# Performance work log

Measured on AMD Instinct MI355X. Metric: run time of the kernel, lower is better.

## Reference

```python
import jax, jax.numpy as jnp
import numpy as np

B, E, T, N = 1024, 512, 8, 256


def setup_inputs() -> dict:
    key = jax.random.key(0)
    k1, k2, k3, k4 = jax.random.split(key, 4)
    weights = jax.random.uniform(k1, (T,), dtype=jnp.float32)  # one scalar per bond type
    bond_src = jax.random.randint(k2, (B, E), 0, N - 1, dtype=jnp.int32)  # raw i, offset +1 later
    bond_dst = jax.random.randint(k3, (B, E), 0, N - 1, dtype=jnp.int32)
    bond_type = jax.random.randint(k4, (B, E), 0, T, dtype=jnp.int32)
    return {"weights": weights, "bond_src": bond_src, "bond_dst": bond_dst,
            "bond_type": bond_type, "num_nodes": N}


def reference(weights, bond_src, bond_dst, bond_type, num_nodes):
    # Gather per-bond weight, then symmetric scatter into dense [B, N, N] adjacency.
    batch, n_edges = bond_src.shape
    w = weights[bond_type]                                  # [B, E] gather
    bidx = jnp.broadcast_to(jnp.arange(batch)[:, None], (batch, n_edges))
    src = bond_src + 1                                      # +1 node offset as in torch code
    dst = bond_dst + 1
    bond_matrix = jnp.zeros((batch, num_nodes, num_nodes), dtype=weights.dtype)
    bond_matrix = bond_matrix.at[bidx, src, dst].set(w)
    bond_matrix = bond_matrix.at[bidx, dst, src].set(w)
    return bond_matrix
```

## Files before the change

### kernel.cpp

```cpp
#include <hip/hip_runtime.h>


#define NB_E 512
#define NB_N 256
#define CH_ROWS 64
#define CH_WORDS (CH_ROWS * NB_N / 2)

typedef float v4f __attribute__((ext_vector_type(4)));

__device__ __forceinline__ void lds_max_u16(unsigned int* tab, int cell, unsigned int v16)
{
    unsigned int* w = tab + (cell >> 1);
    const int sh = (cell & 1) * 16;
    unsigned int old = *w;
    while (true) {
        const unsigned int cur = (old >> sh) & 0xFFFFu;
        if (cur >= v16) break;
        const unsigned int nw = (old & ~(0xFFFFu << sh)) | (v16 << sh);
        const unsigned int seen = atomicCAS(w, old, nw);
        if (seen == old) break;
        old = seen;
    }
}

__global__ __launch_bounds__(256) void BondWeight_41738492182540_kernel(
    const float* __restrict__ weights,
    const int*   __restrict__ bsrc,
    const int*   __restrict__ bdst,
    const int*   __restrict__ btyp,
    float*       __restrict__ out)
{
    __shared__ unsigned int seqtab[CH_WORDS];
    __shared__ float s_wt[8];

    const int b = blockIdx.x;
    const int t = threadIdx.x;

    if (t < 8) s_wt[t] = weights[t];

    const int ebase = b * NB_E;
    int row[4], col[4];
    unsigned int pk[4];
    #pragma unroll
    for (int i = 0; i < 2; ++i) {
        const int e  = t + 256 * i;
        const int s1 = bsrc[ebase + e] + 1;
        const int d1 = bdst[ebase + e] + 1;
        const unsigned int ty = (unsigned int)btyp[ebase + e] & 7u;
        row[2*i]   = s1; col[2*i]   = d1; pk[2*i]   = ((unsigned int)(e + 1) << 3) | ty;
        row[2*i+1] = d1; col[2*i+1] = s1; pk[2*i+1] = ((unsigned int)(NB_E + e + 1) << 3) | ty;
    }

    {
        uint4* tab4 = (uint4*)seqtab;
        #pragma unroll
        for (int k = 0; k < CH_WORDS / 4 / 256; ++k)
            tab4[t + 256 * k] = make_uint4(0u, 0u, 0u, 0u);
    }
    __syncthreads();

    float4* __restrict__ out4 = ((float4*)out) + (size_t)b * (NB_N * NB_N / 4);
    uint2*  __restrict__ tab2 = (uint2*)seqtab;

    for (int r0 = 0; r0 < NB_N; r0 += CH_ROWS) {
        #pragma unroll
        for (int i = 0; i < 4; ++i) {
            const int r = row[i] - r0;
            if (0 <= r && r < CH_ROWS)
                lds_max_u16(seqtab, r * NB_N + col[i], pk[i]);
        }
        __syncthreads();

        #pragma unroll
        for (int k = 0; k < (CH_ROWS * NB_N / 4) / 256; ++k) {
            const int i4 = t + 256 * k;
            const uint2 ab = tab2[i4];
            tab2[i4] = make_uint2(0u, 0u);
            v4f v;
            unsigned int p;
            p = ab.x & 0xFFFFu; v.x = p ? s_wt[p & 7u] : 0.0f;
            p = ab.x >> 16;     v.y = p ? s_wt[p & 7u] : 0.0f;
            p = ab.y & 0xFFFFu; v.z = p ? s_wt[p & 7u] : 0.0f;
            p = ab.y >> 16;     v.w = p ? s_wt[p & 7u] : 0.0f;
            *(v4f*)&out4[r0 * (NB_N / 4) + i4] = v;
        }
        __syncthreads();
    }
}

extern "C" void kernel_launch(void* const* d_in, const int* in_sizes, int n_in,
                              void* d_out, int out_size, void* d_ws, size_t ws_size,
                              hipStream_t stream) {
    const float* weights = (const float*)d_in[0];
    const int*   bsrc    = (const int*)d_in[1];
    const int*   bdst    = (const int*)d_in[2];
    const int*   btyp    = (const int*)d_in[3];
    float*       out     = (float*)d_out;

    const int nb = in_sizes[1] / NB_E;

    BondWeight_41738492182540_kernel<<<nb, 256, 0, stream>>>(
        weights, bsrc, bdst, btyp, out);
}
```

Measured before the change: 272.8 us.

## Split each batch's row chunks across four blocks instead of looping

Launches four blocks per batch, each handling one 64-row chunk of the adjacency matrix, instead of one block looping over four chunks. This increases the number of blocks in flight and removes the per-chunk syncs and the table re-clearing. Edge loads become int2 vector loads with a changed edge-to-thread mapping, and the sequence numbering is kept consistent so the last-write priority is preserved. The cost is that every block re-reads all of its batch's edges, so edge reads from global memory increase fourfold.

Measured after the change: 275.5 us. Within noise of the previous version (+1.0%).

```diff
diff --git a/kernel.cpp b/kernel.cpp
--- a/kernel.cpp
+++ b/kernel.cpp
@@ -33,23 +33,12 @@
     __shared__ unsigned int seqtab[CH_WORDS];
     __shared__ float s_wt[8];
 
-    const int b = blockIdx.x;
-    const int t = threadIdx.x;
+    const int bx = blockIdx.x;
+    const int b  = bx >> 2;
+    const int r0 = (bx & 3) * CH_ROWS;
+    const int t  = threadIdx.x;
 
     if (t < 8) s_wt[t] = weights[t];
-
-    const int ebase = b * NB_E;
-    int row[4], col[4];
-    unsigned int pk[4];
-    #pragma unroll
-    for (int i = 0; i < 2; ++i) {
-        const int e  = t + 256 * i;
-        const int s1 = bsrc[ebase + e] + 1;
-        const int d1 = bdst[ebase + e] + 1;
-        const unsigned int ty = (unsigned int)btyp[ebase + e] & 7u;
-        row[2*i]   = s1; col[2*i]   = d1; pk[2*i]   = ((unsigned int)(e + 1) << 3) | ty;
-        row[2*i+1] = d1; col[2*i+1] = s1; pk[2*i+1] = ((unsigned int)(NB_E + e + 1) << 3) | ty;
-    }
 
     {
         uint4* tab4 = (uint4*)seqtab;
@@ -57,34 +46,51 @@
         for (int k = 0; k < CH_WORDS / 4 / 256; ++k)
             tab4[t + 256 * k] = make_uint4(0u, 0u, 0u, 0u);
     }
+
+    const int2 s2 = ((const int2*)(bsrc + b * NB_E))[t];
+    const int2 d2 = ((const int2*)(bdst + b * NB_E))[t];
+    const int2 y2 = ((const int2*)(btyp + b * NB_E))[t];
+
+    int row[4], col[4];
+    unsigned int pk[4];
+    {
+        const int e0 = 2 * t, e1 = 2 * t + 1;
+        const int sa = s2.x + 1, da = d2.x + 1;
+        const int sb = s2.y + 1, db = d2.y + 1;
+        const unsigned int ta = (unsigned int)y2.x & 7u;
+        const unsigned int tb = (unsigned int)y2.y & 7u;
+        row[0] = sa; col[0] = da; pk[0] = ((unsigned int)(e0 + 1) << 3) | ta;
+        row[1] = sb; col[1] = db; pk[1] = ((unsigned int)(e1 + 1) << 3) | tb;
+        row[2] = da; col[2] = sa; pk[2] = ((unsigned int)(NB_E + e0 + 1) << 3) | ta;
+        row[3] = db; col[3] = sb; pk[3] = ((unsigned int)(NB_E + e1 + 1) << 3) | tb;
+    }
+
     __syncthreads();
 
-    float4* __restrict__ out4 = ((float4*)out) + (size_t)b * (NB_N * NB_N / 4);
-    uint2*  __restrict__ tab2 = (uint2*)seqtab;
+    #pragma unroll
+    for (int i = 0; i < 4; ++i) {
+        const int r = row[i] - r0;
+        if (0 <= r && r < CH_ROWS)
+            lds_max_u16(seqtab, r * NB_N + col[i], pk[i]);
+    }
 
-    for (int r0 = 0; r0 < NB_N; r0 += CH_ROWS) {
-        #pragma unroll
-        for (int i = 0; i < 4; ++i) {
-            const int r = row[i] - r0;
-            if (0 <= r && r < CH_ROWS)
-                lds_max_u16(seqtab, r * NB_N + col[i], pk[i]);
-        }
-        __syncthreads();
+    __syncthreads();
 
-        #pragma unroll
-        for (int k = 0; k < (CH_ROWS * NB_N / 4) / 256; ++k) {
-            const int i4 = t + 256 * k;
-            const uint2 ab = tab2[i4];
-            tab2[i4] = make_uint2(0u, 0u);
-            v4f v;
-            unsigned int p;
-            p = ab.x & 0xFFFFu; v.x = p ? s_wt[p & 7u] : 0.0f;
-            p = ab.x >> 16;     v.y = p ? s_wt[p & 7u] : 0.0f;
-            p = ab.y & 0xFFFFu; v.z = p ? s_wt[p & 7u] : 0.0f;
-            p = ab.y >> 16;     v.w = p ? s_wt[p & 7u] : 0.0f;
-            *(v4f*)&out4[r0 * (NB_N / 4) + i4] = v;
-        }
-        __syncthreads();
+    float4* __restrict__ out4 = ((float4*)out)
+        + (size_t)b * (NB_N * NB_N / 4) + r0 * (NB_N / 4);
+    const uint2* __restrict__ tab2 = (const uint2*)seqtab;
+
+    #pragma unroll
+    for (int k = 0; k < (CH_ROWS * NB_N / 4) / 256; ++k) {
+        const int i4 = t + 256 * k;
+        const uint2 ab = tab2[i4];
+        v4f v;
+        unsigned int p;
+        p = ab.x & 0xFFFFu; v.x = p ? s_wt[p & 7u] : 0.0f;
+        p = ab.x >> 16;     v.y = p ? s_wt[p & 7u] : 0.0f;
+        p = ab.y & 0xFFFFu; v.z = p ? s_wt[p & 7u] : 0.0f;
+        p = ab.y >> 16;     v.w = p ? s_wt[p & 7u] : 0.0f;
+        *(v4f*)&out4[i4] = v;
     }
 }
 
@@ -99,6 +105,6 @@
 
     const int nb = in_sizes[1] / NB_E;
 
-    BondWeight_41738492182540_kernel<<<nb, 256, 0, stream>>>(
+    BondWeight_41738492182540_kernel<<<nb * 4, 256, 0, stream>>>(
         weights, bsrc, bdst, btyp, out);
 }
```
